# Performance work log

Hardware: AMD Instinct MI355X
Metric: run time of the kernel (lower is better)

## Reference

```python
import jax, jax.numpy as jnp
import numpy as np
from jax import lax
from itertools import product

KS = 3          # kernel_size
PAD = 1         # padding
N = KS ** 3     # 27 sample points per voxel


def _conv3d_3x3(x, w, b):
    # x: [b,c,D,H,W], w: [O,c,3,3,3]
    out = lax.conv_general_dilated(x, w, (1, 1, 1), [(PAD, PAD)] * 3,
                                   dimension_numbers=('NCDHW', 'OIDHW', 'NCDHW'))
    return out + b[None, :, None, None, None]


def setup_inputs() -> dict:
    key = jax.random.key(0)
    k1, k2, k3, k4 = jax.random.split(key, 4)
    B, C, D, OUTC = 2, 32, 24, 64
    x = jax.random.normal(k1, (B, C, D, D, D), jnp.float32)
    p_w = jax.random.normal(k2, (3 * N, C, KS, KS, KS), jnp.float32) * 0.02
    p_b = jax.random.normal(k3, (3 * N,), jnp.float32) * 0.02
    conv_w = jax.random.normal(k4, (OUTC, C * N), jnp.float32) / np.sqrt(C * N)
    return {"x": x, "p_w": p_w, "p_b": p_b, "conv_w": conv_w}


def reference(x, p_w, p_b, conv_w):
    b, c, h, w, d = x.shape
    # offset prediction: [b, 3N, h, w, d]
    offset = _conv3d_3x3(x, p_w, p_b)

    # p_n: kernel-relative offsets, p_0: base grid (shifted by +1 for padding)
    r = np.arange(-(KS - 1) // 2, (KS - 1) // 2 + 1)
    gx, gy, gz = np.meshgrid(r, r, r, indexing='ij')
    p_n = jnp.asarray(np.concatenate([gx.ravel(), gy.ravel(), gz.ravel()])
                      .reshape(1, 3 * N, 1, 1, 1), jnp.float32)
    ox, oy, oz = np.meshgrid(np.arange(1, h + 1), np.arange(1, w + 1),
                             np.arange(1, d + 1), indexing='ij')
    def rep(a):
        return np.broadcast_to(a.reshape(1, 1, h, w, d), (1, N, h, w, d))
    p_0 = jnp.asarray(np.concatenate([rep(ox), rep(oy), rep(oz)], axis=1), jnp.float32)

    p = p_0 + p_n + offset                      # [b, 3N, h, w, d]
    p = jnp.transpose(p, (0, 2, 3, 4, 1))        # [b, h, w, d, 3N]

    xp = jnp.pad(x, ((0, 0), (0, 0), (PAD, PAD), (PAD, PAD), (PAD, PAD)))
    sizes = (xp.shape[2], xp.shape[3], xp.shape[4])
    ps = [p[..., :N], p[..., N:2 * N], p[..., 2 * N:]]

    qs, ql, pm = [], [], []
    for ax in range(3):
        s = sizes[ax]
        f = jnp.floor(ps[ax])
        qs.append(jnp.clip(f, 0, s - 1).astype(jnp.int32))
        ql.append(jnp.clip(f + 1, 0, s - 1).astype(jnp.int32))
        # out-of-range mask: snap p to its floor (matches torch detach + floor_p)
        m = lax.stop_gradient(((ps[ax] < PAD) | (ps[ax] > s - 1 - PAD)).astype(ps[ax].dtype))
        pa = ps[ax] * (1 - m) + f * m
        pm.append(jnp.clip(pa, 0, s - 1))

    def gather(xb, qi, qj, qk):
        return xb[:, qi, qj, qk]  # [c, h, w, d, N]

    acc = jnp.zeros((b, c, h, w, d, N), x.dtype)
    for cx, cy, cz in product((0, 1), repeat=3):   # 8 trilinear corners
        bits = (cx, cy, cz)
        q = [qs[a] if bits[a] == 0 else ql[a] for a in range(3)]
        g = jnp.ones_like(pm[0])
        for a in range(3):
            diff = q[a].astype(pm[a].dtype) - pm[a]
            g = g * ((1 + diff) if bits[a] == 0 else (1 - diff))
        xq = jax.vmap(gather)(xp, q[0], q[1], q[2])  # [b, c, h, w, d, N]
        acc = acc + g[:, None] * xq

    # [b,c,h,w,d,N] -> [b, c*N, h, w, d] (c-major, N-minor, as in torch view)
    x_off = jnp.transpose(acc, (0, 1, 5, 2, 3, 4)).reshape(b, c * N, h, w, d)
    out = jnp.einsum('oi,bidhw->bodhw', conv_w, x_off)
    p_out = jnp.concatenate(pm, axis=-1)
    return out, p_out
```

## Files before the change

### kernel.cpp

```cpp
#include <hip/hip_runtime.h>

#define CC 32
#define DIM 24
#define SP (DIM*DIM*DIM)
#define NPTS 27
#define M3 81
#define OUTC 64
#define BATCH 2
#define CN (CC*NPTS)

#define VBB 12
#define NV (NPTS*VBB)
#define CPAD 896
#define MP 84
#define XR 26

typedef __attribute__((ext_vector_type(8))) short short8;
typedef __attribute__((ext_vector_type(4))) float f32x4;

__device__ __forceinline__ unsigned short f2bf(float f) {
    unsigned u = __builtin_bit_cast(unsigned, f);
    return (unsigned short)((u + 0x7FFFu + ((u >> 16) & 1u)) >> 16);
}

__global__ __launch_bounds__(256)
void prep_w_kernel(const float* __restrict__ p_w,
                   const float* __restrict__ conv_w,
                   float* __restrict__ p_wTP,
                   unsigned short* __restrict__ conv_wbf) {
    int id = blockIdx.x * 256 + threadIdx.x;
    if (id < CN * MP) {
        int k = id / MP, m = id % MP;
        p_wTP[id] = (m < M3) ? p_w[(size_t)m * CN + k] : 0.f;
    }
    if (id < CN * OUTC) {
        int o = id / CN, kp = id % CN;
        int n = kp >> 5, c = kp & 31;
        conv_wbf[id] = f2bf(conv_w[(size_t)o * CN + c * NPTS + n]);
    }
}

__global__ __launch_bounds__(256)
void transpose_x_kernel(const float* __restrict__ x,
                        unsigned short* __restrict__ x_t) {
    __shared__ float tile[CC][65];
    int b = blockIdx.x / 216;
    int sp0 = (blockIdx.x % 216) * 64;
    const float* xb = x + (size_t)b * CC * SP;
    for (int it = threadIdx.x; it < CC * 64; it += 256) {
        int c = it >> 6, s = it & 63;
        tile[c][s] = xb[(size_t)c * SP + sp0 + s];
    }
    __syncthreads();
    unsigned short* xtb = x_t + (size_t)b * SP * CC;
    for (int it = threadIdx.x; it < CC * 64; it += 256) {
        int s = it >> 5, c = it & 31;
        xtb[(size_t)(sp0 + s) * CC + c] = f2bf(tile[c][s]);
    }
}

__global__ __launch_bounds__(256, 4)
void offset_gemm_kernel(const float* __restrict__ x,
                        const float* __restrict__ p_wTP,
                        const float* __restrict__ p_b,
                        float* __restrict__ offset) {
    __shared__ float lds[288 * XR];

    int bid = blockIdx.x;
    int j = bid % 24;
    int i = (bid / 24) % 24;
    int b = bid / 576;
    int sp0 = i * 576 + j * 24;
    int t = threadIdx.x;

    for (int it = t; it < 288 * 26; it += 256) {
        int row = it / 26, u = it % 26;
        int c = row / 9, dij = row % 9;
        int di = dij / 3, dj = dij % 3;
        int ii = i + di - 1, jj = j + dj - 1, kk = u - 1;
        bool v = ((unsigned)ii < (unsigned)DIM) && ((unsigned)jj < (unsigned)DIM) &&
                 ((unsigned)kk < (unsigned)DIM);
        lds[it] =
            v ? x[((size_t)(b * CC + c) * SP) + ii * 576 + jj * 24 + kk] : 0.f;
    }
    __syncthreads();

    int w = t >> 6, l = t & 63;
    int mt = l / 3, vt = l % 3;
    bool act = (l < 63);
    if (mt > 20) mt = 20;

    float acc[4][8];
    #pragma unroll
    for (int a = 0; a < 4; ++a)
        #pragma unroll
        for (int e = 0; e < 8; ++e) acc[a][e] = 0.f;

    const float* wbase = p_wTP + (size_t)(w * 216) * MP + mt * 4;
    const float* xbase = lds + (w * 72) * XR + vt * 8;

    float4 pwA[3], pwB[3];
    #pragma unroll
    for (int dk = 0; dk < 3; ++dk)
        pwA[dk] = *(const float4*)(wbase + (size_t)dk * MP);

    #define FMA_BODY(PW, CDIJ)                                              \
        do {                                                                \
            const float* xr = xbase + (CDIJ) * XR;                          \
            float2 x0 = *(const float2*)(xr);                               \
            float2 x1 = *(const float2*)(xr + 2);                           \
            float2 x2 = *(const float2*)(xr + 4);                           \
            float2 x3 = *(const float2*)(xr + 6);                           \
            float2 x4 = *(const float2*)(xr + 8);                           \
            float xv[10] = { x0.x, x0.y, x1.x, x1.y, x2.x, x2.y,            \
                             x3.x, x3.y, x4.x, x4.y };                      \
            _Pragma("unroll")                                               \
            for (int dk = 0; dk < 3; ++dk) {                                \
                float4 wv = PW[dk];                                         \
                _Pragma("unroll")                                           \
                for (int e = 0; e < 8; ++e) {                               \
                    float xvv = xv[dk + e];                                 \
                    acc[0][e] += wv.x * xvv;                                \
                    acc[1][e] += wv.y * xvv;                                \
                    acc[2][e] += wv.z * xvv;                                \
                    acc[3][e] += wv.w * xvv;                                \
                }                                                           \
            }                                                               \
        } while (0)

    for (int cdij = 0; cdij < 72; cdij += 2) {
        {
            const float* wn = wbase + (size_t)((cdij + 1) * 3) * MP;
            #pragma unroll
            for (int dk = 0; dk < 3; ++dk)
                pwB[dk] = *(const float4*)(wn + (size_t)dk * MP);
            __builtin_amdgcn_sched_barrier(0);
            FMA_BODY(pwA, cdij);
        }
        {
            const float* wn = wbase + (size_t)((cdij + 2) * 3) * MP;
            #pragma unroll
            for (int dk = 0; dk < 3; ++dk)
                pwA[dk] = *(const float4*)(wn + (size_t)dk * MP);
            __builtin_amdgcn_sched_barrier(0);
            FMA_BODY(pwB, cdij + 1);
        }
    }
    #undef FMA_BODY
    __syncthreads();

    float* part = lds;
    if (act && w < 2) {
        #pragma unroll
        for (int a = 0; a < 4; ++a) {
            #pragma unroll
            for (int e2 = 0; e2 < 2; ++e2) {
                float4 pv = make_float4(acc[a][e2 * 4], acc[a][e2 * 4 + 1],
                                        acc[a][e2 * 4 + 2], acc[a][e2 * 4 + 3]);
                *(float4*)&part[((w * MP) + mt * 4 + a) * 24 + vt * 8 + e2 * 4] = pv;
            }
        }
    }
    __syncthreads();
    if (act && w >= 2) {
        #pragma unroll
        for (int a = 0; a < 4; ++a) {
            #pragma unroll
            for (int e2 = 0; e2 < 2; ++e2) {
                float* dst = &part[(((w - 2) * MP) + mt * 4 + a) * 24 + vt * 8 + e2 * 4];
                float4 pv = *(const float4*)dst;
                pv.x += acc[a][e2 * 4];     pv.y += acc[a][e2 * 4 + 1];
                pv.z += acc[a][e2 * 4 + 2]; pv.w += acc[a][e2 * 4 + 3];
                *(float4*)dst = pv;
            }
        }
    }
    __syncthreads();

    for (int it = t; it < M3 * 6; it += 256) {
        int m = it / 6, vq = it % 6;
        float4 p0 = *(const float4*)&part[(m) * 24 + vq * 4];
        float4 p1 = *(const float4*)&part[(MP + m) * 24 + vq * 4];
        float bias = p_b[m];
        float4 s = make_float4(p0.x + p1.x + bias, p0.y + p1.y + bias,
                               p0.z + p1.z + bias, p0.w + p1.w + bias);
        *(float4*)&offset[((size_t)(b * M3 + m)) * SP + sp0 + vq * 4] = s;
    }
}

__global__ __launch_bounds__(256, 4)
void sample_gemm_kernel(const unsigned short* __restrict__ x_t,
                        const float* __restrict__ offset,
                        const unsigned short* __restrict__ conv_wbf,
                        float* __restrict__ out,
                        float* __restrict__ p_out) {
    __shared__ __align__(16) unsigned char region[VBB * CPAD * 2 + 8 * NV * 4];
    unsigned short* col = (unsigned short*)region;
    unsigned* s_corner = (unsigned*)(region + VBB * CPAD * 2);

    int bid = blockIdx.x;
    int r = bid & 1;
    int j = (bid >> 1) % 24;
    int i = ((bid >> 1) / 24) % 24;
    int b = bid / 1152;
    int k0 = r * VBB;
    int sp0 = i * 576 + j * 24 + k0;
    int t = threadIdx.x;

    const unsigned short* xtb = x_t + (size_t)b * SP * CC;

    for (int it = t; it < NV; it += 256) {
        int v = it % VBB, n = it / VBB;
        int sp = sp0 + v;
        int k = k0 + v;

        int pnx = n / 9 - 1, pny = (n / 3) % 3 - 1, pnz = n % 3 - 1;
        float p0a[3] = { (float)(i + 1 + pnx),
                         (float)(j + 1 + pny),
                         (float)(k + 1 + pnz) };
        int ql[3], qh[3];
        float wl[3], wh[3];
        #pragma unroll
        for (int ax = 0; ax < 3; ++ax) {
            int m = ax * NPTS + n;
            float p = p0a[ax] + offset[((size_t)(b * M3 + m)) * SP + sp];
            float f = floorf(p);
            int qlo = (int)fminf(fmaxf(f,       0.f), 25.f);
            int qhi = (int)fminf(fmaxf(f + 1.f, 0.f), 25.f);
            bool oob = (p < 1.f) || (p > 24.f);
            float pa = oob ? f : p;
            float pm = fminf(fmaxf(pa, 0.f), 25.f);
            ql[ax] = qlo; qh[ax] = qhi;
            wl[ax] = 1.f + ((float)qlo - pm);
            wh[ax] = 1.f - ((float)qhi - pm);
            p_out[((size_t)(b * SP + sp)) * M3 + m] = pm;
        }

        #pragma unroll
        for (int cr = 0; cr < 8; ++cr) {
            int ii = ((cr & 4) ? qh[0] : ql[0]) - 1;
            int jj = ((cr & 2) ? qh[1] : ql[1]) - 1;
            int kk = ((cr & 1) ? qh[2] : ql[2]) - 1;
            bool valid = ((unsigned)ii < (unsigned)DIM) &&
                         ((unsigned)jj < (unsigned)DIM) &&
                         ((unsigned)kk < (unsigned)DIM);
            float cw = ((cr & 4) ? wh[0] : wl[0]) *
                       ((cr & 2) ? wh[1] : wl[1]) *
                       ((cr & 1) ? wh[2] : wl[2]);
            unsigned idx = (unsigned)(ii * 576 + jj * 24 + kk);
            s_corner[cr * NV + it] =
                valid ? ((idx << 16) | (unsigned)f2bf(cw)) : 0u;
        }
    }
    __syncthreads();

    for (int task = t; task < NV * 4; task += 256) {
        int item = task >> 2, q = task & 3;
        int v = item % VBB, n = item / VBB;

        const unsigned short* xq = xtb + q * 8;
        float acc[8];
        #pragma unroll
        for (int e = 0; e < 8; ++e) acc[e] = 0.f;

        #pragma unroll
        for (int cr = 0; cr < 8; ++cr) {
            unsigned u = s_corner[cr * NV + item];
            float wc = __builtin_bit_cast(float, u << 16);
            const unsigned* s = (const unsigned*)(xq + (size_t)(u >> 16) * CC);
            #pragma unroll
            for (int q2 = 0; q2 < 4; ++q2) {
                unsigned uu = s[q2];
                acc[2 * q2]     += wc * __builtin_bit_cast(float, uu << 16);
                acc[2 * q2 + 1] += wc * __builtin_bit_cast(float, uu & 0xFFFF0000u);
            }
        }

        short8 pk;
        #pragma unroll
        for (int e = 0; e < 8; ++e)
            pk[e] = (short)f2bf(acc[e]);
        int sv = (v & 7) << 3;
        *(short8*)&col[v * CPAD + ((n * 32 + q * 8) ^ sv)] = pk;
    }
    __syncthreads();

    {
        int mt = t >> 6;
        int l = t & 63;
        int lr = l & 15;
        int g = l >> 4;
        int sv = (lr & 7) << 3;

        const short8* ap =
            (const short8*)(conv_wbf + ((size_t)(mt * 16 + lr)) * CN + g * 8);
        const unsigned short* bp = col + lr * CPAD;

        f32x4 acc = {0.f, 0.f, 0.f, 0.f};
        #pragma unroll 3
        for (int kb = 0; kb < CN / 32; ++kb) {
            short8 a = ap[kb * 4];
            short8 bb = *(const short8*)&bp[(kb * 32 + g * 8) ^ sv];
            acc = __builtin_amdgcn_mfma_f32_16x16x32_bf16(a, bb, acc, 0, 0, 0);
        }
        if (lr < VBB) {
            float* op = out + ((size_t)(b * OUTC + mt * 16 + g * 4)) * SP + sp0 + lr;
            #pragma unroll
            for (int rr = 0; rr < 4; ++rr)
                op[(size_t)rr * SP] = acc[rr];
        }
    }
}

extern "C" void kernel_launch(void* const* d_in, const int* in_sizes, int n_in,
                              void* d_out, int out_size, void* d_ws, size_t ws_size,
                              hipStream_t stream) {
    const float* x      = (const float*)d_in[0];
    const float* p_w    = (const float*)d_in[1];
    const float* p_b    = (const float*)d_in[2];
    const float* conv_w = (const float*)d_in[3];

    float* out_all = (float*)d_out;
    float* out_main = out_all;
    float* p_out    = out_all + (size_t)BATCH * OUTC * SP;

    float* offset          = (float*)d_ws;
    float* p_wTP           = offset + (size_t)BATCH * M3 * SP;
    unsigned short* conv_wbf = (unsigned short*)(p_wTP + (size_t)CN * MP);
    unsigned short* x_t    = conv_wbf + (size_t)CN * OUTC;

    {
        int total = CN * MP;
        prep_w_kernel<<<(total + 255) / 256, 256, 0, stream>>>(p_w, conv_w,
                                                               p_wTP, conv_wbf);
    }
    {
        int blocks = BATCH * (SP / 64);
        transpose_x_kernel<<<blocks, 256, 0, stream>>>(x, x_t);
    }
    {
        int blocks = BATCH * 24 * 24;
        offset_gemm_kernel<<<blocks, 256, 0, stream>>>(x, p_wTP, p_b, offset);
    }
    {
        int blocks = BATCH * 24 * 24 * 2;
        sample_gemm_kernel<<<blocks, 256, 0, stream>>>(x_t, offset, conv_wbf,
                                                       out_main, p_out);
    }
}
```

Before: 118.0 us.

## Stream offset-conv weights into LDS with double-buffered direct global-to-LDS loads

Replaces the per-thread register prefetch of offset weights with per-wave global_load_lds transfers into a double-buffered LDS chunk. Each wave copies 252 floats per step and the FMA loop then reads weights from LDS, which removes redundant global loads and frees VGPRs. There is no barrier between waves, only s_waitcnt, so correctness depends on the direct-to-LDS writes being visible within the wave. It also adds LDS usage and an LDS read per dk that can contend with the x halo reads. The last iteration also loads past the 216 rows into the neighbouring wave's region or past the buffer end, which is harmless only if that memory is in bounds.

```diff
diff --git a/kernel.cpp b/kernel.cpp
--- a/kernel.cpp
+++ b/kernel.cpp
@@ -14,6 +14,8 @@
 #define CPAD 896
 #define MP 84
 #define XR 26
+#define HALOF (288*XR)
+#define CHUNKF 256
 
 typedef __attribute__((ext_vector_type(8))) short short8;
 typedef __attribute__((ext_vector_type(4))) float f32x4;
@@ -21,6 +23,12 @@
 __device__ __forceinline__ unsigned short f2bf(float f) {
     unsigned u = __builtin_bit_cast(unsigned, f);
     return (unsigned short)((u + 0x7FFFu + ((u >> 16) & 1u)) >> 16);
+}
+
+__device__ __forceinline__ void gload16(const float* g, float* l) {
+    __builtin_amdgcn_global_load_lds(
+        (const __attribute__((address_space(1))) void*)g,
+        (__attribute__((address_space(3))) void*)l, 16, 0, 0);
 }
 
 __global__ __launch_bounds__(256)
@@ -64,7 +72,7 @@
                         const float* __restrict__ p_wTP,
                         const float* __restrict__ p_b,
                         float* __restrict__ offset) {
-    __shared__ float lds[288 * XR];
+    __shared__ __align__(16) float lds[HALOF + 4 * 2 * CHUNKF];
 
     int bid = blockIdx.x;
     int j = bid % 24;
@@ -96,15 +104,11 @@
         #pragma unroll
         for (int e = 0; e < 8; ++e) acc[a][e] = 0.f;
 
-    const float* wbase = p_wTP + (size_t)(w * 216) * MP + mt * 4;
+    const float* gw = p_wTP + (size_t)(w * 216) * MP;
     const float* xbase = lds + (w * 72) * XR + vt * 8;
-
-    float4 pwA[3], pwB[3];
-    #pragma unroll
-    for (int dk = 0; dk < 3; ++dk)
-        pwA[dk] = *(const float4*)(wbase + (size_t)dk * MP);
-
-    #define FMA_BODY(PW, CDIJ)                                              \
+    float* cbase = lds + HALOF + w * 2 * CHUNKF;
+
+    #define FMA_BODY(WB, CDIJ)                                              \
         do {                                                                \
             const float* xr = xbase + (CDIJ) * XR;                          \
             float2 x0 = *(const float2*)(xr);                               \
@@ -116,7 +120,7 @@
                              x3.x, x3.y, x4.x, x4.y };                      \
             _Pragma("unroll")                                               \
             for (int dk = 0; dk < 3; ++dk) {                                \
-                float4 wv = PW[dk];                                         \
+                float4 wv = *(const float4*)((WB) + dk * MP);               \
                 _Pragma("unroll")                                           \
                 for (int e = 0; e < 8; ++e) {                               \
                     float xvv = xv[dk + e];                                 \
@@ -128,25 +132,20 @@
             }                                                               \
         } while (0)
 
-    for (int cdij = 0; cdij < 72; cdij += 2) {
-        {
-            const float* wn = wbase + (size_t)((cdij + 1) * 3) * MP;
-            #pragma unroll
-            for (int dk = 0; dk < 3; ++dk)
-                pwB[dk] = *(const float4*)(wn + (size_t)dk * MP);
-            __builtin_amdgcn_sched_barrier(0);
-            FMA_BODY(pwA, cdij);
-        }
-        {
-            const float* wn = wbase + (size_t)((cdij + 2) * 3) * MP;
-            #pragma unroll
-            for (int dk = 0; dk < 3; ++dk)
-                pwA[dk] = *(const float4*)(wn + (size_t)dk * MP);
-            __builtin_amdgcn_sched_barrier(0);
-            FMA_BODY(pwB, cdij + 1);
-        }
+    gload16(gw + l * 4, cbase);
+
+    int cur = 0;
+    for (int cdij = 0; cdij < 72; ++cdij) {
+        gload16(gw + (size_t)(cdij + 1) * 252 + l * 4,
+                cbase + (cur ^ 1) * CHUNKF);
+        asm volatile("s_waitcnt vmcnt(1)" ::: "memory");
+        __builtin_amdgcn_sched_barrier(0);
+        FMA_BODY(cbase + cur * CHUNKF + mt * 4, cdij);
+        cur ^= 1;
     }
     #undef FMA_BODY
+    asm volatile("s_waitcnt vmcnt(0)" ::: "memory");
+    __builtin_amdgcn_sched_barrier(0);
     __syncthreads();
 
     float* part = lds;
```

After: 132.7 us. 1.12x slower.
